# Kernel tuning notes

Measured on AMD Instinct MI355X. Metric: run time of the kernel, lower is better.

Reference implementation:

```python
import jax, jax.numpy as jnp
import numpy as np

B, L, T = 64, 256, 800
NMEL, PRE, ARNN, DRNN, ENC, ATT, NF, K = 80, 256, 512, 512, 512, 128, 32, 31
ZP = 0.1  # zoneout prob (eval-mode expected-value interpolation)


def setup_inputs() -> dict:
    key = jax.random.key(0)
    ks = iter(jax.random.split(key, 32))
    def p(shape, s=0.05):
        return jax.random.normal(next(ks), shape, dtype=jnp.float32) * s
    inp = {
        'encoder_out': jax.random.normal(next(ks), (B, L, ENC), dtype=jnp.float32),
        'lengths': jax.random.randint(next(ks), (B,), L // 2, L + 1),
        'mels': jax.random.normal(next(ks), (B, T, NMEL), dtype=jnp.float32),
        # prenet: 3 bias-free linears with relu (eval: dropout off)
        'Wp1': p((PRE, NMEL)), 'Wp2': p((PRE, PRE)), 'Wp3': p((PRE, PRE)),
        # attention LSTMCell: input = prenet_dim + enc = 768
        'aWih': p((4 * ARNN, PRE + ENC)), 'aWhh': p((4 * ARNN, ARNN)),
        'abih': jnp.zeros((4 * ARNN,)), 'abhh': jnp.zeros((4 * ARNN,)),
        # decoder LSTMCell: input = att_rnn + enc = 1024
        'dWih': p((4 * DRNN, ARNN + ENC)), 'dWhh': p((4 * DRNN, DRNN)),
        'dbih': jnp.zeros((4 * DRNN,)), 'dbhh': jnp.zeros((4 * DRNN,)),
        # location-sensitive attention (all bias-free)
        'Wq': p((ATT, ARNN)), 'Wm': p((ATT, ENC)),
        'Wconv': p((NF, 2, K)), 'Wloc': p((ATT, NF)), 'v': p((1, ATT)),
        # output projection + gate
        'Wout': p((NMEL, DRNN + ENC)), 'bout': jnp.zeros((NMEL,)),
        'Wgate': p((1, DRNN + ENC)), 'bgate': jnp.zeros((1,)),
    }
    return inp


def _lstm(x, h, c, Wih, Whh, bih, bhh):
    g = x @ Wih.T + h @ Whh.T + (bih + bhh)
    i, f, gg, o = jnp.split(g, 4, axis=-1)
    c2 = jax.nn.sigmoid(f) * c + jax.nn.sigmoid(i) * jnp.tanh(gg)
    return jax.nn.sigmoid(o) * jnp.tanh(c2), c2


def _zoneout(new, old):
    return ZP * old + (1.0 - ZP) * new


def decoder_forward(encoder_out, lengths, mels, Wp1, Wp2, Wp3,
                    aWih, aWhh, abih, abhh, dWih, dWhh, dbih, dbhh,
                    Wq, Wm, Wconv, Wloc, v, Wout, bout, Wgate, bgate):
    b, l, _ = encoder_out.shape
    t = mels.shape[1]
    processed_memory = encoder_out @ Wm.T                       # (B,L,ATT)
    mask = jnp.arange(l)[None, :] >= lengths[:, None]           # True = padded
    # teacher forcing inputs: shift mels right by one zero frame
    dec_in = jnp.concatenate(
        [jnp.zeros((b, 1, NMEL), encoder_out.dtype), mels[:, :t - 1]], axis=1)
    xs = jnp.swapaxes(dec_in, 0, 1)                             # (T,B,NMEL)

    def step(carry, frame):
        ah, ac, dh, dc, ctx, aw, aws = carry
        x = jax.nn.relu(jax.nn.relu(jax.nn.relu(frame @ Wp1.T) @ Wp2.T) @ Wp3.T)
        ah2, ac2 = _lstm(jnp.concatenate([x, ctx], -1), ah, ac, aWih, aWhh, abih, abhh)
        ah2, ac2 = _zoneout(ah2, ah), _zoneout(ac2, ac)
        # location features: conv over (B,2,L)
        aw_cat = jnp.stack([aw, aws], axis=1)
        loc = jax.lax.conv_general_dilated(
            aw_cat, Wconv, window_strides=(1,), padding=[((K - 1) // 2,) * 2],
            dimension_numbers=('NCH', 'OIH', 'NCH'))                # (B,NF,L)
        ploc = jnp.swapaxes(loc, 1, 2) @ Wloc.T                      # (B,L,ATT)
        e = jnp.tanh(ah2[:, None, :] @ Wq.T + processed_memory + ploc)
        energies = jnp.squeeze(e @ v.T, -1)                          # (B,L)
        energies = jnp.where(mask, jnp.float32(-1e9), energies)
        w = jax.nn.softmax(energies, axis=-1)
        ctx2 = jnp.einsum('bl,ble->be', w, encoder_out)
        aws2 = aws + w
        dh2, dc2 = _lstm(jnp.concatenate([ah2, ctx2], -1), dh, dc, dWih, dWhh, dbih, dbhh)
        dh2, dc2 = _zoneout(dh2, dh), _zoneout(dc2, dc)
        dhc = jnp.concatenate([dh2, ctx2], axis=-1)
        mel = dhc @ Wout.T + bout
        gate = jnp.squeeze(dhc @ Wgate.T + bgate, -1)
        return (ah2, ac2, dh2, dc2, ctx2, w, aws2), (mel, gate, w)

    z = lambda *s: jnp.zeros(s, encoder_out.dtype)
    carry0 = (z(b, ARNN), z(b, ARNN), z(b, DRNN), z(b, DRNN), z(b, ENC), z(b, l), z(b, l))
    _, (mel_t, gate_t, align_t) = jax.lax.scan(step, carry0, xs)
    return (jnp.swapaxes(mel_t, 0, 1),      # (B,T,NMEL)
            jnp.swapaxes(gate_t, 0, 1),     # (B,T)
            jnp.swapaxes(align_t, 0, 1))    # (B,T,L)


def reference(encoder_out, lengths, mels, Wp1, Wp2, Wp3,
              aWih, aWhh, abih, abhh, dWih, dWhh, dbih, dbhh,
              Wq, Wm, Wconv, Wloc, v, Wout, bout, Wgate, bgate):
    return decoder_forward(encoder_out, lengths, mels, Wp1, Wp2, Wp3,
                           aWih, aWhh, abih, abhh, dWih, dWhh, dbih, dbhh,
                           Wq, Wm, Wconv, Wloc, v, Wout, bout, Wgate, bgate)
```

## Files before the change

kernel.cpp:

```cpp
#include <hip/hip_runtime.h>


#define DEV_INLINE __device__ __forceinline__

constexpr int TB = 800;

constexpr size_t PMT_O = 0;
constexpr size_t GDT_O = 2097152;
constexpr size_t ENG_O = 2228224;
constexpr size_t WQT_O = 2244608;
constexpr size_t AH_O  = 2310144;
constexpr size_t AC_O  = 2375680;
constexpr size_t DH_O  = 2441216;
constexpr size_t DC_O  = 2506752;
constexpr size_t CTX_O = 2572288;
constexpr size_t AW_O  = 2637824;
constexpr size_t AWS_O = 2670592;
constexpr size_t XB_O  = 2703360;

constexpr size_t MEL_O  = 0;
constexpr size_t GATE_O = 4096000;
constexpr size_t ALG_O  = 4147200;

DEV_INLINE float sigf(float x)     { return 1.0f / (1.0f + __expf(-x)); }
DEV_INLINE float tanhfast(float x) { float e = __expf(2.0f * x); return 1.0f - 2.0f / (e + 1.0f); }

template<int NO>
DEV_INLINE void gseg(float* __restrict__ acc,
                     const float* __restrict__ inT,
                     const float* __restrict__ W, const int ldw, const int wcol0,
                     const int* __restrict__ rows, const int segk0, const int seglen,
                     const int ks, const int ke, const int lane)
{
  const int a0 = ks > segk0 ? ks : segk0;
  const int a1 = (ke < segk0 + seglen) ? ke : (segk0 + seglen);
  if (a0 >= a1) return;
  const float* __restrict__ ip = inT + (size_t)(a0 - segk0) * 64 + lane;
  const int n = a1 - a0;
  const float* wp[NO];
#pragma unroll
  for (int j = 0; j < NO; ++j)
    wp[j] = W + (size_t)rows[j] * ldw + (wcol0 + (a0 - segk0));
  for (int k = 0; k < n; k += 4) {
    const float x0 = ip[(k + 0) * 64];
    const float x1 = ip[(k + 1) * 64];
    const float x2 = ip[(k + 2) * 64];
    const float x3 = ip[(k + 3) * 64];
#pragma unroll
    for (int j = 0; j < NO; ++j)
      acc[j] += x0 * wp[j][k] + x1 * wp[j][k + 1] + x2 * wp[j][k + 2] + x3 * wp[j][k + 3];
  }
}

__global__ __launch_bounds__(256) void init_kernel(const float* __restrict__ Wq,
                                                   float* __restrict__ ws)
{
  const int i = blockIdx.x * 256 + threadIdx.x;
  {
    const int k = i >> 7, a = i & 127;
    ws[WQT_O + i] = Wq[a * 512 + k];
  }
  for (size_t idx = i; idx < 393216; idx += 65536)
    ws[AH_O + idx] = 0.0f;
}

__global__ __launch_bounds__(256) void prenet_kernel(const float* __restrict__ mels,
                                                     const float* __restrict__ Wp1,
                                                     const float* __restrict__ Wp2,
                                                     const float* __restrict__ Wp3,
                                                     float* __restrict__ xb, int t0)
{
  __shared__ float smem[16384];
  const int t = t0 + blockIdx.x;
  const int tid = threadIdx.x;
  const int lane = tid & 63;
  const int wv = __builtin_amdgcn_readfirstlane(tid >> 6);

  if (t == 0) {
    for (int i = tid; i < 5200; i += 256) smem[i] = 0.0f;
  } else {
    for (int i = tid; i < 5120; i += 256) {
      const int b = i / 80, k = i - b * 80;
      smem[k * 65 + b] = mels[((size_t)b * TB + (t - 1)) * 80 + k];
    }
  }
  __syncthreads();

  float va[8][8];
#pragma unroll
  for (int g = 0; g < 8; ++g) {
    const int u0 = wv * 64 + g * 8;
    float acc[8] = {};
    for (int k = 0; k < 80; ++k) {
      const float x = smem[k * 65 + lane];
#pragma unroll
      for (int j = 0; j < 8; ++j) acc[j] += x * Wp1[(u0 + j) * 80 + k];
    }
#pragma unroll
    for (int j = 0; j < 8; ++j) va[g][j] = fmaxf(acc[j], 0.0f);
  }
  __syncthreads();
#pragma unroll
  for (int g = 0; g < 8; ++g)
#pragma unroll
    for (int j = 0; j < 8; ++j) smem[(wv * 64 + g * 8 + j) * 64 + lane] = va[g][j];
  __syncthreads();

#pragma unroll
  for (int g = 0; g < 8; ++g) {
    const int u0 = wv * 64 + g * 8;
    float acc[8] = {};
    for (int k = 0; k < 256; ++k) {
      const float x = smem[k * 64 + lane];
#pragma unroll
      for (int j = 0; j < 8; ++j) acc[j] += x * Wp2[(u0 + j) * 256 + k];
    }
#pragma unroll
    for (int j = 0; j < 8; ++j) va[g][j] = fmaxf(acc[j], 0.0f);
  }
  __syncthreads();
#pragma unroll
  for (int g = 0; g < 8; ++g)
#pragma unroll
    for (int j = 0; j < 8; ++j) smem[(wv * 64 + g * 8 + j) * 64 + lane] = va[g][j];
  __syncthreads();

#pragma unroll
  for (int g = 0; g < 8; ++g) {
    const int u0 = wv * 64 + g * 8;
    float acc[8] = {};
    for (int k = 0; k < 256; ++k) {
      const float x = smem[k * 64 + lane];
#pragma unroll
      for (int j = 0; j < 8; ++j) acc[j] += x * Wp3[(u0 + j) * 256 + k];
    }
#pragma unroll
    for (int j = 0; j < 8; ++j)
      xb[((size_t)blockIdx.x * 256 + (u0 + j)) * 64 + lane] = fmaxf(acc[j], 0.0f);
  }
}

__global__ __launch_bounds__(256) void pm_kernel(const float* __restrict__ enc,
                                                 const float* __restrict__ Wm,
                                                 float* __restrict__ pmT)
{
  __shared__ float encL[64 * 129];
  const int b = blockIdx.x >> 2;
  const int l0 = (blockIdx.x & 3) * 64;
  const int tid = threadIdx.x;
  const int lane = tid & 63;
  const int wv = __builtin_amdgcn_readfirstlane(tid >> 6);

  float acc[4][8];
#pragma unroll
  for (int ai = 0; ai < 4; ++ai)
#pragma unroll
    for (int j = 0; j < 8; ++j) acc[ai][j] = 0.0f;

  for (int kc = 0; kc < 4; ++kc) {
    __syncthreads();
    for (int i = tid; i < 64 * 128; i += 256) {
      const int l = i >> 7, k = i & 127;
      encL[l * 129 + k] = enc[((size_t)b * 256 + l0 + l) * 512 + kc * 128 + k];
    }
    __syncthreads();
#pragma unroll
    for (int ai = 0; ai < 4; ++ai) {
      const int agrp = (ai * 4 + wv) * 8;
      for (int k = 0; k < 128; ++k) {
        const float x = encL[lane * 129 + k];
#pragma unroll
        for (int j = 0; j < 8; ++j)
          acc[ai][j] += x * Wm[(size_t)(agrp + j) * 512 + kc * 128 + k];
      }
    }
  }
#pragma unroll
  for (int ai = 0; ai < 4; ++ai) {
    const int agrp = (ai * 4 + wv) * 8;
#pragma unroll
    for (int j = 0; j < 8; ++j)
      pmT[((size_t)b * 128 + agrp + j) * 256 + l0 + lane] = acc[ai][j];
  }
}

__global__ __launch_bounds__(256) void k_alstm(
    const float* __restrict__ xt,  const float* __restrict__ ctx_i,
    const float* __restrict__ ah_i, const float* __restrict__ ac_i,
    float* __restrict__ ah_o, float* __restrict__ ac_o,
    const float* __restrict__ dh_i,
    const float* __restrict__ aWih, const float* __restrict__ aWhh,
    const float* __restrict__ abih, const float* __restrict__ abhh,
    const float* __restrict__ Wout, const float* __restrict__ bout,
    const float* __restrict__ Wgate, const float* __restrict__ bgate,
    float* __restrict__ out, int t, int do_a, int do_m)
{
  __shared__ float sm[2048];
  const int tid = threadIdx.x;
  const int blk = blockIdx.x;
  const int lane = tid & 63;
  const int wv = __builtin_amdgcn_readfirstlane(tid >> 6);

  if (blk < 256) {
    if (!do_a) return;
    const int u0 = blk * 2;
    int rows[8];
#pragma unroll
    for (int j = 0; j < 8; ++j) rows[j] = u0 + (j >> 2) + 512 * (j & 3);
    float acc[8] = {};
    const int ks = wv * 320, ke = ks + 320;
    gseg<8>(acc, xt,    aWih, 768, 0,   rows, 0,   256, ks, ke, lane);
    gseg<8>(acc, ctx_i, aWih, 768, 256, rows, 256, 512, ks, ke, lane);
    gseg<8>(acc, ah_i,  aWhh, 512, 0,   rows, 768, 512, ks, ke, lane);
#pragma unroll
    for (int j = 0; j < 8; ++j) sm[(wv * 8 + j) * 64 + lane] = acc[j];
    __syncthreads();
    if (tid < 128) {
      const int m = tid & 63, uq = tid >> 6;
      const int u = u0 + uq;
      float g[4];
#pragma unroll
      for (int q = 0; q < 4; ++q) {
        const int j = uq * 4 + q;
        const int row = u + 512 * q;
        g[q] = sm[j * 64 + m] + sm[(8 + j) * 64 + m] + sm[(16 + j) * 64 + m] + sm[(24 + j) * 64 + m]
             + abih[row] + abhh[row];
      }
      const float co = ac_i[u * 64 + m], ho = ah_i[u * 64 + m];
      const float c2 = sigf(g[1]) * co + sigf(g[0]) * tanhfast(g[2]);
      const float h2 = sigf(g[3]) * tanhfast(c2);
      ah_o[u * 64 + m] = 0.1f * ho + 0.9f * h2;
      ac_o[u * 64 + m] = 0.1f * co + 0.9f * c2;
    }
  } else if (do_m && blk < 277) {
    if (blk < 276) {
      const int c0 = (blk - 256) * 4;
      int rows[4] = {c0, c0 + 1, c0 + 2, c0 + 3};
      float acc[4] = {};
      const int ks = wv * 256, ke = ks + 256;
      gseg<4>(acc, dh_i,  Wout, 1024, 0,   rows, 0,   512, ks, ke, lane);
      gseg<4>(acc, ctx_i, Wout, 1024, 512, rows, 512, 512, ks, ke, lane);
#pragma unroll
      for (int j = 0; j < 4; ++j) sm[(wv * 4 + j) * 64 + lane] = acc[j];
      __syncthreads();
      {
        const int m = tid & 63, c = tid >> 6;
        const float val = sm[c * 64 + m] + sm[(4 + c) * 64 + m] + sm[(8 + c) * 64 + m] + sm[(12 + c) * 64 + m]
                        + bout[c0 + c];
        out[MEL_O + ((size_t)m * TB + (t - 1)) * 80 + c0 + c] = val;
      }
    } else {
      float acc[1] = {};
      int rows1[1] = {0};
      const int ks = wv * 256, ke = ks + 256;
      gseg<1>(acc, dh_i,  Wgate, 1024, 0,   rows1, 0,   512, ks, ke, lane);
      gseg<1>(acc, ctx_i, Wgate, 1024, 512, rows1, 512, 512, ks, ke, lane);
      sm[wv * 64 + lane] = acc[0];
      __syncthreads();
      if (tid < 64) {
        const float val = sm[tid] + sm[64 + tid] + sm[128 + tid] + sm[192 + tid] + bgate[0];
        out[GATE_O + (size_t)tid * TB + (t - 1)] = val;
      }
    }
  }
}

__global__ __launch_bounds__(256) void k_energy(
    const float* __restrict__ ah2,  const float* __restrict__ dh_i,
    const float* __restrict__ aw_i, const float* __restrict__ aws_i,
    const float* __restrict__ pmT,  const float* __restrict__ wqT,
    float* __restrict__ gdT, float* __restrict__ eng,
    const float* __restrict__ dWih, const float* __restrict__ dWhh,
    const float* __restrict__ dbih, const float* __restrict__ dbhh,
    const float* __restrict__ Wconv, const float* __restrict__ Wloc,
    const float* __restrict__ v, const int* __restrict__ len)
{
  __shared__ float sm[3584];
  const int tid = threadIdx.x;
  const int blk = blockIdx.x;
  const int lane = tid & 63;
  const int wv = __builtin_amdgcn_readfirstlane(tid >> 6);

  if (blk < 256) {
    const int u0 = blk * 2;
    int rows[8];
#pragma unroll
    for (int j = 0; j < 8; ++j) rows[j] = u0 + (j >> 2) + 512 * (j & 3);
    float acc[8] = {};
    const int ks = wv * 256, ke = ks + 256;
    gseg<8>(acc, ah2,  dWih, 1024, 0, rows, 0,   512, ks, ke, lane);
    gseg<8>(acc, dh_i, dWhh, 512,  0, rows, 512, 512, ks, ke, lane);
#pragma unroll
    for (int j = 0; j < 8; ++j) sm[(wv * 8 + j) * 64 + lane] = acc[j];
    __syncthreads();
    if (tid < 128) {
      const int m = tid & 63, uq = tid >> 6;
      const int u = u0 + uq;
#pragma unroll
      for (int q = 0; q < 4; ++q) {
        const int j = uq * 4 + q;
        const int row = u + 512 * q;
        gdT[(size_t)row * 64 + m] =
            sm[j * 64 + m] + sm[(8 + j) * 64 + m] + sm[(16 + j) * 64 + m] + sm[(24 + j) * 64 + m]
          + dbih[row] + dbhh[row];
      }
    }
  } else {
    const int eb = blk - 256;
    const int b = eb >> 2;
    const int l0 = (eb & 3) * 64;
    float* qL   = sm;
    float* a2L  = sm + 128;
    float* awL  = sm + 640;
    float* awsL = sm + 928;
    float* locL = sm + 1216;
    float* pr   = sm + 3328;

    for (int k = tid; k < 512; k += 256) a2L[k] = ah2[(size_t)k * 64 + b];
    if (tid < 15) { awL[tid] = 0.0f; awsL[tid] = 0.0f; awL[271 + tid] = 0.0f; awsL[271 + tid] = 0.0f; }
    awL[15 + tid]  = aw_i[b * 256 + tid];
    awsL[15 + tid] = aws_i[b * 256 + tid];
    __syncthreads();
    {
      const int a = tid & 127, h = tid >> 7;
      float qp = 0.0f;
      const float* wq = wqT + (size_t)(h * 256) * 128 + a;
      const float* xv = a2L + h * 256;
      for (int k = 0; k < 256; k += 4)
        qp += wq[(k + 0) * 128] * xv[k + 0] + wq[(k + 1) * 128] * xv[k + 1]
            + wq[(k + 2) * 128] * xv[k + 2] + wq[(k + 3) * 128] * xv[k + 3];
      locL[h * 128 + a] = qp;
    }
    __syncthreads();
    if (tid < 128) qL[tid] = locL[tid] + locL[128 + tid];
    __syncthreads();
    {
      float awv[31], awsv[31];
#pragma unroll
      for (int k = 0; k < 31; ++k) { awv[k] = awL[l0 + lane + k]; awsv[k] = awsL[l0 + lane + k]; }
      const int f0 = wv * 8;
      for (int f = f0; f < f0 + 8; ++f) {
        const float* wc = Wconv + f * 62;
        float lf = 0.0f;
#pragma unroll
        for (int k = 0; k < 31; ++k) lf += awv[k] * wc[k] + awsv[k] * wc[31 + k];
        locL[lane * 33 + f] = lf;
      }
    }
    __syncthreads();
    {
      float locv[32];
#pragma unroll
      for (int f = 0; f < 32; ++f) locv[f] = locL[lane * 33 + f];
      float part = 0.0f;
      const int a0 = wv * 32;
      const float* pmp = pmT + (size_t)b * 128 * 256 + l0 + lane;
      for (int a = a0; a < a0 + 32; ++a) {
        float s = qL[a] + pmp[(size_t)a * 256];
        const float* wl = Wloc + a * 32;
#pragma unroll
        for (int f = 0; f < 32; ++f) s += locv[f] * wl[f];
        part += v[a] * tanhfast(s);
      }
      pr[wv * 64 + lane] = part;
    }
    __syncthreads();
    if (tid < 64) {
      float e = pr[tid] + pr[64 + tid] + pr[128 + tid] + pr[192 + tid];
      const int l = l0 + tid;
      if (l >= len[b]) e = -1e9f;
      eng[b * 256 + l] = e;
    }
  }
}

__global__ __launch_bounds__(256) void k_ctx(
    const float* __restrict__ eng, const float* __restrict__ enc,
    const float* __restrict__ aws_i,
    float* __restrict__ ctx_o, float* __restrict__ aw_o, float* __restrict__ aws_o,
    float* __restrict__ out, int t)
{
  __shared__ float sm[896];
  const int tid = threadIdx.x;
  const int lane = tid & 63;
  const int wv = __builtin_amdgcn_readfirstlane(tid >> 6);
  const int b = blockIdx.x >> 2;
  const int ec = blockIdx.x & 3;
  const int e0 = ec * 128;
  float* eL = sm;
  float* wL = sm + 256;
  float* red = sm + 512;
  float* partL = sm + 640;

  eL[tid] = eng[b * 256 + tid];
  __syncthreads();
  float vv = eL[tid];
  for (int mm = 32; mm >= 1; mm >>= 1) vv = fmaxf(vv, __shfl_xor(vv, mm, 64));
  if (lane == 0) red[wv] = vv;
  __syncthreads();
  const float mx = fmaxf(fmaxf(red[0], red[1]), fmaxf(red[2], red[3]));
  const float pex = __expf(eL[tid] - mx);
  wL[tid] = pex;
  float ss = pex;
  for (int mm = 32; mm >= 1; mm >>= 1) ss += __shfl_xor(ss, mm, 64);
  if (lane == 0) red[4 + wv] = ss;
  __syncthreads();
  const float inv = 1.0f / (red[4] + red[5] + red[6] + red[7]);
  {
    const int e_i = tid & 127, lh = tid >> 7;
    float cp = 0.0f;
    const float* ep = enc + ((size_t)b * 256 + lh * 128) * 512 + e0 + e_i;
    for (int l = 0; l < 128; ++l) cp += wL[lh * 128 + l] * ep[(size_t)l * 512];
    partL[lh * 128 + e_i] = cp;
  }
  __syncthreads();
  if (tid < 128) ctx_o[(size_t)(e0 + tid) * 64 + b] = (partL[tid] + partL[128 + tid]) * inv;
  if (ec == 0) {
    const float w = wL[tid] * inv;
    aw_o[b * 256 + tid] = w;
    aws_o[b * 256 + tid] = aws_i[b * 256 + tid] + w;
    out[ALG_O + ((size_t)b * TB + t) * 256 + tid] = w;
  }
}

__global__ __launch_bounds__(256) void k_dfin(
    const float* __restrict__ ctx_o, const float* __restrict__ gdT,
    const float* __restrict__ dh_i,  const float* __restrict__ dc_i,
    float* __restrict__ dh_o, float* __restrict__ dc_o,
    const float* __restrict__ dWih)
{
  __shared__ float sm[2048];
  const int tid = threadIdx.x;
  const int lane = tid & 63;
  const int wv = __builtin_amdgcn_readfirstlane(tid >> 6);
  const int u0 = blockIdx.x * 2;
  int rows[8];
#pragma unroll
  for (int j = 0; j < 8; ++j) rows[j] = u0 + (j >> 2) + 512 * (j & 3);
  float acc[8] = {};
  const int ks = wv * 128, ke = ks + 128;
  gseg<8>(acc, ctx_o, dWih, 1024, 512, rows, 0, 512, ks, ke, lane);
#pragma unroll
  for (int j = 0; j < 8; ++j) sm[(wv * 8 + j) * 64 + lane] = acc[j];
  __syncthreads();
  if (tid < 128) {
    const int m = tid & 63, uq = tid >> 6;
    const int u = u0 + uq;
    float g[4];
#pragma unroll
    for (int q = 0; q < 4; ++q) {
      const int j = uq * 4 + q;
      const int row = u + 512 * q;
      g[q] = sm[j * 64 + m] + sm[(8 + j) * 64 + m] + sm[(16 + j) * 64 + m] + sm[(24 + j) * 64 + m]
           + gdT[(size_t)row * 64 + m];
    }
    const float co = dc_i[u * 64 + m], ho = dh_i[u * 64 + m];
    const float c2 = sigf(g[1]) * co + sigf(g[0]) * tanhfast(g[2]);
    const float h2 = sigf(g[3]) * tanhfast(c2);
    dh_o[u * 64 + m] = 0.1f * ho + 0.9f * h2;
    dc_o[u * 64 + m] = 0.1f * co + 0.9f * c2;
  }
}

extern "C" void kernel_launch(void* const* d_in, const int* in_sizes, int n_in,
                              void* d_out, int out_size, void* d_ws, size_t ws_size,
                              hipStream_t stream)
{
  (void)in_sizes; (void)n_in; (void)out_size;
  const float* enc   = (const float*)d_in[0];
  const int*   len   = (const int*)  d_in[1];
  const float* mels  = (const float*)d_in[2];
  const float* Wp1   = (const float*)d_in[3];
  const float* Wp2   = (const float*)d_in[4];
  const float* Wp3   = (const float*)d_in[5];
  const float* aWih  = (const float*)d_in[6];
  const float* aWhh  = (const float*)d_in[7];
  const float* abih  = (const float*)d_in[8];
  const float* abhh  = (const float*)d_in[9];
  const float* dWih  = (const float*)d_in[10];
  const float* dWhh  = (const float*)d_in[11];
  const float* dbih  = (const float*)d_in[12];
  const float* dbhh  = (const float*)d_in[13];
  const float* Wq    = (const float*)d_in[14];
  const float* Wm    = (const float*)d_in[15];
  const float* Wconv = (const float*)d_in[16];
  const float* Wloc  = (const float*)d_in[17];
  const float* vv    = (const float*)d_in[18];
  const float* Wout  = (const float*)d_in[19];
  const float* bout  = (const float*)d_in[20];
  const float* Wgate = (const float*)d_in[21];
  const float* bgate = (const float*)d_in[22];

  float* ws  = (float*)d_ws;
  float* out = (float*)d_out;

  const size_t need_big = (XB_O + (size_t)TB * 16384) * 4;
  const int CH = (ws_size >= need_big) ? TB : 64;

  init_kernel<<<256, 256, 0, stream>>>(Wq, ws);
  pm_kernel<<<256, 256, 0, stream>>>(enc, Wm, ws + PMT_O);

  for (int t = 0; t <= TB; ++t) {
    if (t < TB && (t % CH) == 0) {
      const int nt = (TB - t) < CH ? (TB - t) : CH;
      prenet_kernel<<<nt, 256, 0, stream>>>(mels, Wp1, Wp2, Wp3, ws + XB_O, t);
    }
    const int cur = t & 1;
    const float* xt = ws + XB_O + (size_t)(t % CH) * 16384;
    float* ah_i = ws + AH_O  + (size_t)cur * 32768;  float* ah_o = ws + AH_O  + (size_t)(cur ^ 1) * 32768;
    float* ac_i = ws + AC_O  + (size_t)cur * 32768;  float* ac_o = ws + AC_O  + (size_t)(cur ^ 1) * 32768;
    float* dh_i = ws + DH_O  + (size_t)cur * 32768;  float* dh_o = ws + DH_O  + (size_t)(cur ^ 1) * 32768;
    float* dc_i = ws + DC_O  + (size_t)cur * 32768;  float* dc_o = ws + DC_O  + (size_t)(cur ^ 1) * 32768;
    float* ctx_i = ws + CTX_O + (size_t)cur * 32768; float* ctx_o = ws + CTX_O + (size_t)(cur ^ 1) * 32768;
    float* aw_i = ws + AW_O  + (size_t)cur * 16384;  float* aw_o = ws + AW_O  + (size_t)(cur ^ 1) * 16384;
    float* aws_i = ws + AWS_O + (size_t)cur * 16384; float* aws_o = ws + AWS_O + (size_t)(cur ^ 1) * 16384;

    k_alstm<<<277, 256, 0, stream>>>(xt, ctx_i, ah_i, ac_i, ah_o, ac_o, dh_i,
                                     aWih, aWhh, abih, abhh,
                                     Wout, bout, Wgate, bgate,
                                     out, t, (t < TB) ? 1 : 0, (t > 0) ? 1 : 0);
    if (t == TB) break;
    k_energy<<<512, 256, 0, stream>>>(ah_o, dh_i, aw_i, aws_i,
                                      ws + PMT_O, ws + WQT_O, ws + GDT_O, ws + ENG_O,
                                      dWih, dWhh, dbih, dbhh, Wconv, Wloc, vv, len);
    k_ctx<<<256, 256, 0, stream>>>(ws + ENG_O, enc, aws_i, ctx_o, aw_o, aws_o, out, t);
    k_dfin<<<256, 256, 0, stream>>>(ctx_o, ws + GDT_O, dh_i, dc_i, dh_o, dc_o, dWih);
  }
}
```

Before: 87.46 ms.

## Replace per-step kernel launches with a persistent kernel using grid barriers

Swaps the roughly 3200 per-timestep kernel launches for one persistent 256-block kernel. Its blocks split the work by role (attention LSTM, decoder gates, energy and context, mel and gate, prenet stages) and meet at a software global barrier built on an atomic counter, two barriers per step. The prenet is now computed one step ahead inside the loop instead of as a bulk precompute, and the location-conv features are staged separately. This targets launch overhead and inter-kernel gaps on a latency-bound recurrence. It relies on all 256 blocks being co-resident and adds atomic spin-wait cost at every barrier.

```diff
diff --git a/kernel.cpp b/kernel.cpp
--- a/kernel.cpp
+++ b/kernel.cpp
@@ -5,18 +5,22 @@
 
 constexpr int TB = 800;
 
-constexpr size_t PMT_O = 0;
-constexpr size_t GDT_O = 2097152;
-constexpr size_t ENG_O = 2228224;
-constexpr size_t WQT_O = 2244608;
-constexpr size_t AH_O  = 2310144;
-constexpr size_t AC_O  = 2375680;
-constexpr size_t DH_O  = 2441216;
-constexpr size_t DC_O  = 2506752;
-constexpr size_t CTX_O = 2572288;
-constexpr size_t AW_O  = 2637824;
-constexpr size_t AWS_O = 2670592;
-constexpr size_t XB_O  = 2703360;
+constexpr size_t PMT_O  = 0;
+constexpr size_t GDT_O  = 2097152;
+constexpr size_t WQT_O  = 2228224;
+constexpr size_t LOCF_O = 2293760;
+constexpr size_t Y1_O   = 2818048;
+constexpr size_t Y2_O   = 2834432;
+constexpr size_t XR_O   = 2850816;
+constexpr size_t AH_O   = 2883584;
+constexpr size_t AC_O   = 2949120;
+constexpr size_t DH_O   = 3014656;
+constexpr size_t DC_O   = 3080192;
+constexpr size_t CTX_O  = 3145728;
+constexpr size_t AW_O   = 3211264;
+constexpr size_t AWS_O  = 3244032;
+constexpr size_t BAR_O  = 3276800;
+constexpr size_t ZERO_N = 983296;
 
 constexpr size_t MEL_O  = 0;
 constexpr size_t GATE_O = 4096000;
@@ -24,6 +28,28 @@
 
 DEV_INLINE float sigf(float x)     { return 1.0f / (1.0f + __expf(-x)); }
 DEV_INLINE float tanhfast(float x) { float e = __expf(2.0f * x); return 1.0f - 2.0f / (e + 1.0f); }
+
+struct Params {
+  const float* enc; const int* len; const float* mels;
+  const float* Wp1; const float* Wp2; const float* Wp3;
+  const float* aWih; const float* aWhh; const float* abih; const float* abhh;
+  const float* dWih; const float* dWhh; const float* dbih; const float* dbhh;
+  const float* Wconv; const float* Wloc; const float* v;
+  const float* Wout; const float* bout; const float* Wgate; const float* bgate;
+  float* ws; float* out;
+};
+
+DEV_INLINE void gbar(unsigned* cnt, unsigned target)
+{
+  __syncthreads();
+  __threadfence();
+  if (threadIdx.x == 0) {
+    atomicAdd(cnt, 1u);
+    while (atomicAdd(cnt, 0u) < target) __builtin_amdgcn_s_sleep(8);
+  }
+  __syncthreads();
+  __threadfence();
+}
 
 template<int NO>
 DEV_INLINE void gseg(float* __restrict__ acc,
@@ -60,18 +86,18 @@
     const int k = i >> 7, a = i & 127;
     ws[WQT_O + i] = Wq[a * 512 + k];
   }
-  for (size_t idx = i; idx < 393216; idx += 65536)
-    ws[AH_O + idx] = 0.0f;
+  for (size_t idx = i; idx < ZERO_N; idx += 65536)
+    ws[LOCF_O + idx] = 0.0f;
 }
 
 __global__ __launch_bounds__(256) void prenet_kernel(const float* __restrict__ mels,
                                                      const float* __restrict__ Wp1,
                                                      const float* __restrict__ Wp2,
                                                      const float* __restrict__ Wp3,
-                                                     float* __restrict__ xb, int t0)
+                                                     float* __restrict__ xb)
 {
   __shared__ float smem[16384];
-  const int t = t0 + blockIdx.x;
+  const int t = blockIdx.x;
   const int tid = threadIdx.x;
   const int lane = tid & 63;
   const int wv = __builtin_amdgcn_readfirstlane(tid >> 6);
@@ -136,7 +162,7 @@
     }
 #pragma unroll
     for (int j = 0; j < 8; ++j)
-      xb[((size_t)blockIdx.x * 256 + (u0 + j)) * 64 + lane] = fmaxf(acc[j], 0.0f);
+      xb[((size_t)t * 256 + (u0 + j)) * 64 + lane] = fmaxf(acc[j], 0.0f);
   }
 }
 
@@ -184,262 +210,71 @@
   }
 }
 
-__global__ __launch_bounds__(256) void k_alstm(
-    const float* __restrict__ xt,  const float* __restrict__ ctx_i,
-    const float* __restrict__ ah_i, const float* __restrict__ ac_i,
-    float* __restrict__ ah_o, float* __restrict__ ac_o,
-    const float* __restrict__ dh_i,
-    const float* __restrict__ aWih, const float* __restrict__ aWhh,
-    const float* __restrict__ abih, const float* __restrict__ abhh,
-    const float* __restrict__ Wout, const float* __restrict__ bout,
-    const float* __restrict__ Wgate, const float* __restrict__ bgate,
-    float* __restrict__ out, int t, int do_a, int do_m)
-{
-  __shared__ float sm[2048];
-  const int tid = threadIdx.x;
-  const int blk = blockIdx.x;
-  const int lane = tid & 63;
-  const int wv = __builtin_amdgcn_readfirstlane(tid >> 6);
-
-  if (blk < 256) {
-    if (!do_a) return;
-    const int u0 = blk * 2;
-    int rows[8];
-#pragma unroll
-    for (int j = 0; j < 8; ++j) rows[j] = u0 + (j >> 2) + 512 * (j & 3);
-    float acc[8] = {};
-    const int ks = wv * 320, ke = ks + 320;
-    gseg<8>(acc, xt,    aWih, 768, 0,   rows, 0,   256, ks, ke, lane);
-    gseg<8>(acc, ctx_i, aWih, 768, 256, rows, 256, 512, ks, ke, lane);
-    gseg<8>(acc, ah_i,  aWhh, 512, 0,   rows, 768, 512, ks, ke, lane);
-#pragma unroll
-    for (int j = 0; j < 8; ++j) sm[(wv * 8 + j) * 64 + lane] = acc[j];
-    __syncthreads();
-    if (tid < 128) {
-      const int m = tid & 63, uq = tid >> 6;
-      const int u = u0 + uq;
-      float g[4];
-#pragma unroll
-      for (int q = 0; q < 4; ++q) {
-        const int j = uq * 4 + q;
-        const int row = u + 512 * q;
-        g[q] = sm[j * 64 + m] + sm[(8 + j) * 64 + m] + sm[(16 + j) * 64 + m] + sm[(24 + j) * 64 + m]
-             + abih[row] + abhh[row];
-      }
-      const float co = ac_i[u * 64 + m], ho = ah_i[u * 64 + m];
-      const float c2 = sigf(g[1]) * co + sigf(g[0]) * tanhfast(g[2]);
-      const float h2 = sigf(g[3]) * tanhfast(c2);
-      ah_o[u * 64 + m] = 0.1f * ho + 0.9f * h2;
-      ac_o[u * 64 + m] = 0.1f * co + 0.9f * c2;
-    }
-  } else if (do_m && blk < 277) {
-    if (blk < 276) {
-      const int c0 = (blk - 256) * 4;
-      int rows[4] = {c0, c0 + 1, c0 + 2, c0 + 3};
-      float acc[4] = {};
-      const int ks = wv * 256, ke = ks + 256;
-      gseg<4>(acc, dh_i,  Wout, 1024, 0,   rows, 0,   512, ks, ke, lane);
-      gseg<4>(acc, ctx_i, Wout, 1024, 512, rows, 512, 512, ks, ke, lane);
-#pragma unroll
-      for (int j = 0; j < 4; ++j) sm[(wv * 4 + j) * 64 + lane] = acc[j];
-      __syncthreads();
-      {
-        const int m = tid & 63, c = tid >> 6;
-        const float val = sm[c * 64 + m] + sm[(4 + c) * 64 + m] + sm[(8 + c) * 64 + m] + sm[(12 + c) * 64 + m]
-                        + bout[c0 + c];
-        out[MEL_O + ((size_t)m * TB + (t - 1)) * 80 + c0 + c] = val;
-      }
-    } else {
-      float acc[1] = {};
-      int rows1[1] = {0};
-      const int ks = wv * 256, ke = ks + 256;
-      gseg<1>(acc, dh_i,  Wgate, 1024, 0,   rows1, 0,   512, ks, ke, lane);
-      gseg<1>(acc, ctx_i, Wgate, 1024, 512, rows1, 512, 512, ks, ke, lane);
-      sm[wv * 64 + lane] = acc[0];
-      __syncthreads();
-      if (tid < 64) {
-        const float val = sm[tid] + sm[64 + tid] + sm[128 + tid] + sm[192 + tid] + bgate[0];
-        out[GATE_O + (size_t)tid * TB + (t - 1)] = val;
-      }
-    }
-  }
-}
-
-__global__ __launch_bounds__(256) void k_energy(
-    const float* __restrict__ ah2,  const float* __restrict__ dh_i,
-    const float* __restrict__ aw_i, const float* __restrict__ aws_i,
-    const float* __restrict__ pmT,  const float* __restrict__ wqT,
-    float* __restrict__ gdT, float* __restrict__ eng,
-    const float* __restrict__ dWih, const float* __restrict__ dWhh,
-    const float* __restrict__ dbih, const float* __restrict__ dbhh,
-    const float* __restrict__ Wconv, const float* __restrict__ Wloc,
-    const float* __restrict__ v, const int* __restrict__ len)
-{
-  __shared__ float sm[3584];
-  const int tid = threadIdx.x;
-  const int blk = blockIdx.x;
-  const int lane = tid & 63;
-  const int wv = __builtin_amdgcn_readfirstlane(tid >> 6);
-
-  if (blk < 256) {
-    const int u0 = blk * 2;
-    int rows[8];
-#pragma unroll
-    for (int j = 0; j < 8; ++j) rows[j] = u0 + (j >> 2) + 512 * (j & 3);
-    float acc[8] = {};
-    const int ks = wv * 256, ke = ks + 256;
-    gseg<8>(acc, ah2,  dWih, 1024, 0, rows, 0,   512, ks, ke, lane);
-    gseg<8>(acc, dh_i, dWhh, 512,  0, rows, 512, 512, ks, ke, lane);
-#pragma unroll
-    for (int j = 0; j < 8; ++j) sm[(wv * 8 + j) * 64 + lane] = acc[j];
-    __syncthreads();
-    if (tid < 128) {
-      const int m = tid & 63, uq = tid >> 6;
-      const int u = u0 + uq;
-#pragma unroll
-      for (int q = 0; q < 4; ++q) {
-        const int j = uq * 4 + q;
-        const int row = u + 512 * q;
-        gdT[(size_t)row * 64 + m] =
-            sm[j * 64 + m] + sm[(8 + j) * 64 + m] + sm[(16 + j) * 64 + m] + sm[(24 + j) * 64 + m]
-          + dbih[row] + dbhh[row];
-      }
-    }
-  } else {
-    const int eb = blk - 256;
-    const int b = eb >> 2;
-    const int l0 = (eb & 3) * 64;
-    float* qL   = sm;
-    float* a2L  = sm + 128;
-    float* awL  = sm + 640;
-    float* awsL = sm + 928;
-    float* locL = sm + 1216;
-    float* pr   = sm + 3328;
-
-    for (int k = tid; k < 512; k += 256) a2L[k] = ah2[(size_t)k * 64 + b];
-    if (tid < 15) { awL[tid] = 0.0f; awsL[tid] = 0.0f; awL[271 + tid] = 0.0f; awsL[271 + tid] = 0.0f; }
-    awL[15 + tid]  = aw_i[b * 256 + tid];
-    awsL[15 + tid] = aws_i[b * 256 + tid];
-    __syncthreads();
-    {
-      const int a = tid & 127, h = tid >> 7;
-      float qp = 0.0f;
-      const float* wq = wqT + (size_t)(h * 256) * 128 + a;
-      const float* xv = a2L + h * 256;
-      for (int k = 0; k < 256; k += 4)
-        qp += wq[(k + 0) * 128] * xv[k + 0] + wq[(k + 1) * 128] * xv[k + 1]
-            + wq[(k + 2) * 128] * xv[k + 2] + wq[(k + 3) * 128] * xv[k + 3];
-      locL[h * 128 + a] = qp;
-    }
-    __syncthreads();
-    if (tid < 128) qL[tid] = locL[tid] + locL[128 + tid];
-    __syncthreads();
-    {
-      float awv[31], awsv[31];
-#pragma unroll
-      for (int k = 0; k < 31; ++k) { awv[k] = awL[l0 + lane + k]; awsv[k] = awsL[l0 + lane + k]; }
-      const int f0 = wv * 8;
-      for (int f = f0; f < f0 + 8; ++f) {
-        const float* wc = Wconv + f * 62;
-        float lf = 0.0f;
-#pragma unroll
-        for (int k = 0; k < 31; ++k) lf += awv[k] * wc[k] + awsv[k] * wc[31 + k];
-        locL[lane * 33 + f] = lf;
-      }
-    }
-    __syncthreads();
-    {
-      float locv[32];
-#pragma unroll
-      for (int f = 0; f < 32; ++f) locv[f] = locL[lane * 33 + f];
-      float part = 0.0f;
-      const int a0 = wv * 32;
-      const float* pmp = pmT + (size_t)b * 128 * 256 + l0 + lane;
-      for (int a = a0; a < a0 + 32; ++a) {
-        float s = qL[a] + pmp[(size_t)a * 256];
-        const float* wl = Wloc + a * 32;
-#pragma unroll
-        for (int f = 0; f < 32; ++f) s += locv[f] * wl[f];
-        part += v[a] * tanhfast(s);
-      }
-      pr[wv * 64 + lane] = part;
-    }
-    __syncthreads();
-    if (tid < 64) {
-      float e = pr[tid] + pr[64 + tid] + pr[128 + tid] + pr[192 + tid];
-      const int l = l0 + tid;
-      if (l >= len[b]) e = -1e9f;
-      eng[b * 256 + l] = e;
-    }
-  }
-}
-
-__global__ __launch_bounds__(256) void k_ctx(
-    const float* __restrict__ eng, const float* __restrict__ enc,
-    const float* __restrict__ aws_i,
-    float* __restrict__ ctx_o, float* __restrict__ aw_o, float* __restrict__ aws_o,
-    float* __restrict__ out, int t)
-{
-  __shared__ float sm[896];
-  const int tid = threadIdx.x;
-  const int lane = tid & 63;
-  const int wv = __builtin_amdgcn_readfirstlane(tid >> 6);
-  const int b = blockIdx.x >> 2;
-  const int ec = blockIdx.x & 3;
-  const int e0 = ec * 128;
-  float* eL = sm;
-  float* wL = sm + 256;
-  float* red = sm + 512;
-  float* partL = sm + 640;
-
-  eL[tid] = eng[b * 256 + tid];
-  __syncthreads();
-  float vv = eL[tid];
-  for (int mm = 32; mm >= 1; mm >>= 1) vv = fmaxf(vv, __shfl_xor(vv, mm, 64));
-  if (lane == 0) red[wv] = vv;
-  __syncthreads();
-  const float mx = fmaxf(fmaxf(red[0], red[1]), fmaxf(red[2], red[3]));
-  const float pex = __expf(eL[tid] - mx);
-  wL[tid] = pex;
-  float ss = pex;
-  for (int mm = 32; mm >= 1; mm >>= 1) ss += __shfl_xor(ss, mm, 64);
-  if (lane == 0) red[4 + wv] = ss;
-  __syncthreads();
-  const float inv = 1.0f / (red[4] + red[5] + red[6] + red[7]);
-  {
-    const int e_i = tid & 127, lh = tid >> 7;
-    float cp = 0.0f;
-    const float* ep = enc + ((size_t)b * 256 + lh * 128) * 512 + e0 + e_i;
-    for (int l = 0; l < 128; ++l) cp += wL[lh * 128 + l] * ep[(size_t)l * 512];
-    partL[lh * 128 + e_i] = cp;
-  }
-  __syncthreads();
-  if (tid < 128) ctx_o[(size_t)(e0 + tid) * 64 + b] = (partL[tid] + partL[128 + tid]) * inv;
-  if (ec == 0) {
-    const float w = wL[tid] * inv;
-    aw_o[b * 256 + tid] = w;
-    aws_o[b * 256 + tid] = aws_i[b * 256 + tid] + w;
-    out[ALG_O + ((size_t)b * TB + t) * 256 + tid] = w;
-  }
-}
-
-__global__ __launch_bounds__(256) void k_dfin(
-    const float* __restrict__ ctx_o, const float* __restrict__ gdT,
-    const float* __restrict__ dh_i,  const float* __restrict__ dc_i,
-    float* __restrict__ dh_o, float* __restrict__ dc_o,
-    const float* __restrict__ dWih)
-{
-  __shared__ float sm[2048];
-  const int tid = threadIdx.x;
-  const int lane = tid & 63;
-  const int wv = __builtin_amdgcn_readfirstlane(tid >> 6);
-  const int u0 = blockIdx.x * 2;
+
+DEV_INLINE void f_alstm(int u, int tid, int lane, int wv,
+                        const float* __restrict__ xt, const float* __restrict__ ctx,
+                        const float* __restrict__ ah_i, const float* __restrict__ ac_i,
+                        float* __restrict__ ah_o, float* __restrict__ ac_o,
+                        const Params& p, float* sm)
+{
+  int rows[4] = {u, u + 512, u + 1024, u + 1536};
+  float acc[4] = {};
+  const int ks = wv * 320, ke = ks + 320;
+  gseg<4>(acc, xt,   p.aWih, 768, 0,   rows, 0,   256, ks, ke, lane);
+  gseg<4>(acc, ctx,  p.aWih, 768, 256, rows, 256, 512, ks, ke, lane);
+  gseg<4>(acc, ah_i, p.aWhh, 512, 0,   rows, 768, 512, ks, ke, lane);
+#pragma unroll
+  for (int j = 0; j < 4; ++j) sm[(wv * 4 + j) * 64 + lane] = acc[j];
+  __syncthreads();
+  if (tid < 64) {
+    const int m = tid;
+    float g[4];
+#pragma unroll
+    for (int q = 0; q < 4; ++q)
+      g[q] = sm[q * 64 + m] + sm[(4 + q) * 64 + m] + sm[(8 + q) * 64 + m] + sm[(12 + q) * 64 + m]
+           + p.abih[u + 512 * q] + p.abhh[u + 512 * q];
+    const float co = ac_i[u * 64 + m], ho = ah_i[u * 64 + m];
+    const float c2 = sigf(g[1]) * co + sigf(g[0]) * tanhfast(g[2]);
+    const float h2 = sigf(g[3]) * tanhfast(c2);
+    ah_o[u * 64 + m] = 0.1f * ho + 0.9f * h2;
+    ac_o[u * 64 + m] = 0.1f * co + 0.9f * c2;
+  }
+}
+
+DEV_INLINE void f_dgates(int u, int tid, int lane, int wv,
+                         const float* __restrict__ ah, const float* __restrict__ dh,
+                         float* __restrict__ gdT, const Params& p, float* sm)
+{
+  int rows[4] = {u, u + 512, u + 1024, u + 1536};
+  float acc[4] = {};
+  const int ks = wv * 256, ke = ks + 256;
+  gseg<4>(acc, ah, p.dWih, 1024, 0, rows, 0,   512, ks, ke, lane);
+  gseg<4>(acc, dh, p.dWhh, 512,  0, rows, 512, 512, ks, ke, lane);
+#pragma unroll
+  for (int j = 0; j < 4; ++j) sm[(wv * 4 + j) * 64 + lane] = acc[j];
+  __syncthreads();
+  if (tid < 64) {
+    const int m = tid;
+#pragma unroll
+    for (int q = 0; q < 4; ++q)
+      gdT[(size_t)(u + 512 * q) * 64 + m] =
+          sm[q * 64 + m] + sm[(4 + q) * 64 + m] + sm[(8 + q) * 64 + m] + sm[(12 + q) * 64 + m]
+        + p.dbih[u + 512 * q] + p.dbhh[u + 512 * q];
+  }
+}
+
+DEV_INLINE void f_dfin(int u0, int tid, int lane, int wv,
+                       const float* __restrict__ ctx, const float* __restrict__ gdT,
+                       const float* __restrict__ dh_p, const float* __restrict__ dc_p,
+                       float* __restrict__ dh_o, float* __restrict__ dc_o,
+                       const Params& p, float* sm)
+{
   int rows[8];
 #pragma unroll
   for (int j = 0; j < 8; ++j) rows[j] = u0 + (j >> 2) + 512 * (j & 3);
   float acc[8] = {};
   const int ks = wv * 128, ke = ks + 128;
-  gseg<8>(acc, ctx_o, dWih, 1024, 512, rows, 0, 512, ks, ke, lane);
+  gseg<8>(acc, ctx, p.dWih, 1024, 512, rows, 0, 512, ks, ke, lane);
 #pragma unroll
   for (int j = 0; j < 8; ++j) sm[(wv * 8 + j) * 64 + lane] = acc[j];
   __syncthreads();
@@ -450,11 +285,10 @@
 #pragma unroll
     for (int q = 0; q < 4; ++q) {
       const int j = uq * 4 + q;
-      const int row = u + 512 * q;
       g[q] = sm[j * 64 + m] + sm[(8 + j) * 64 + m] + sm[(16 + j) * 64 + m] + sm[(24 + j) * 64 + m]
-           + gdT[(size_t)row * 64 + m];
-    }
-    const float co = dc_i[u * 64 + m], ho = dh_i[u * 64 + m];
+           + gdT[(size_t)(u + 512 * q) * 64 + m];
+    }
+    const float co = dc_p[u * 64 + m], ho = dh_p[u * 64 + m];
     const float c2 = sigf(g[1]) * co + sigf(g[0]) * tanhfast(g[2]);
     const float h2 = sigf(g[3]) * tanhfast(c2);
     dh_o[u * 64 + m] = 0.1f * ho + 0.9f * h2;
@@ -462,68 +296,297 @@
   }
 }
 
+DEV_INLINE void f_mel(int c0, int tid, int lane, int wv, int tm1,
+                      const float* __restrict__ dh, const float* __restrict__ ctx,
+                      const Params& p, float* sm)
+{
+  int rows[4] = {c0, c0 + 1, c0 + 2, c0 + 3};
+  float acc[4] = {};
+  const int ks = wv * 256, ke = ks + 256;
+  gseg<4>(acc, dh,  p.Wout, 1024, 0,   rows, 0,   512, ks, ke, lane);
+  gseg<4>(acc, ctx, p.Wout, 1024, 512, rows, 512, 512, ks, ke, lane);
+#pragma unroll
+  for (int j = 0; j < 4; ++j) sm[(wv * 4 + j) * 64 + lane] = acc[j];
+  __syncthreads();
+  {
+    const int m = tid & 63, c = tid >> 6;
+    const float val = sm[c * 64 + m] + sm[(4 + c) * 64 + m] + sm[(8 + c) * 64 + m] + sm[(12 + c) * 64 + m]
+                    + p.bout[c0 + c];
+    p.out[MEL_O + ((size_t)m * TB + tm1) * 80 + c0 + c] = val;
+  }
+}
+
+DEV_INLINE void f_gate(int tid, int lane, int wv, int tm1,
+                       const float* __restrict__ dh, const float* __restrict__ ctx,
+                       const Params& p, float* sm)
+{
+  float acc[1] = {};
+  int rows1[1] = {0};
+  const int ks = wv * 256, ke = ks + 256;
+  gseg<1>(acc, dh,  p.Wgate, 1024, 0,   rows1, 0,   512, ks, ke, lane);
+  gseg<1>(acc, ctx, p.Wgate, 1024, 512, rows1, 512, 512, ks, ke, lane);
+  sm[wv * 64 + lane] = acc[0];
+  __syncthreads();
+  if (tid < 64) {
+    const float val = sm[tid] + sm[64 + tid] + sm[128 + tid] + sm[192 + tid] + p.bgate[0];
+    p.out[GATE_O + (size_t)tid * TB + tm1] = val;
+  }
+}
+
+DEV_INLINE void f_conv(int b, int tid,
+                       const float* __restrict__ aw, const float* __restrict__ aws,
+                       float* __restrict__ locF, const Params& p, float* sm)
+{
+  float* awL  = sm;
+  float* awsL = sm + 290;
+  if (tid < 15) { awL[tid] = 0.0f; awsL[tid] = 0.0f; awL[271 + tid] = 0.0f; awsL[271 + tid] = 0.0f; }
+  awL[15 + tid]  = aw[b * 256 + tid];
+  awsL[15 + tid] = aws[b * 256 + tid];
+  __syncthreads();
+  float awv[31], awsv[31];
+#pragma unroll
+  for (int k = 0; k < 31; ++k) { awv[k] = awL[tid + k]; awsv[k] = awsL[tid + k]; }
+  float* dst = locF + ((size_t)b * 256 + tid) * 32;
+  for (int f = 0; f < 32; ++f) {
+    const float* wc = p.Wconv + f * 62;
+    float lf = 0.0f;
+#pragma unroll
+    for (int k = 0; k < 31; ++k) lf += awv[k] * wc[k] + awsv[k] * wc[31 + k];
+    dst[f] = lf;
+  }
+  __syncthreads();
+}
+
+DEV_INLINE void f_energy(int b, int t, int tid, int lane, int wv,
+                         const float* __restrict__ ah, const float* __restrict__ aws_p,
+                         float* __restrict__ ctx_o, float* __restrict__ aw_o,
+                         float* __restrict__ aws_o,
+                         const float* __restrict__ pmT, const float* __restrict__ wqT,
+                         const float* __restrict__ locF, const Params& p, float* sm)
+{
+  float* ahL = sm;
+  float* qpL = sm + 512;
+  float* qL  = sm + 768;
+  float* red = sm + 896;
+  float* wL  = sm + 912;
+  ahL[tid]       = ah[(size_t)tid * 64 + b];
+  ahL[tid + 256] = ah[(size_t)(tid + 256) * 64 + b];
+  __syncthreads();
+  {
+    const int a = tid & 127, h = tid >> 7;
+    float qp = 0.0f;
+    const float* wq = wqT + (size_t)(h * 256) * 128 + a;
+    const float* xv = ahL + h * 256;
+    for (int k = 0; k < 256; k += 4)
+      qp += wq[(k + 0) * 128] * xv[k + 0] + wq[(k + 1) * 128] * xv[k + 1]
+          + wq[(k + 2) * 128] * xv[k + 2] + wq[(k + 3) * 128] * xv[k + 3];
+    qpL[tid] = qp;
+  }
+  __syncthreads();
+  if (tid < 128) qL[tid] = qpL[tid] + qpL[128 + tid];
+  __syncthreads();
+
+  float locv[32];
+  {
+    const float4* lf4 = (const float4*)(locF + ((size_t)b * 256 + tid) * 32);
+#pragma unroll
+    for (int i = 0; i < 8; ++i) {
+      float4 x = lf4[i];
+      locv[4*i] = x.x; locv[4*i+1] = x.y; locv[4*i+2] = x.z; locv[4*i+3] = x.w;
+    }
+  }
+  float part = 0.0f;
+  const float* pmp = pmT + (size_t)b * 32768 + tid;
+#pragma unroll 2
+  for (int a = 0; a < 128; ++a) {
+    float s = qL[a] + pmp[(size_t)a * 256];
+    const float* wl = p.Wloc + a * 32;
+#pragma unroll
+    for (int f = 0; f < 32; ++f) s += locv[f] * wl[f];
+    part += p.v[a] * tanhfast(s);
+  }
+  if (tid >= p.len[b]) part = -1e9f;
+
+  float mv = part;
+  for (int mm = 32; mm >= 1; mm >>= 1) mv = fmaxf(mv, __shfl_xor(mv, mm, 64));
+  if (lane == 0) red[wv] = mv;
+  __syncthreads();
+  const float mx = fmaxf(fmaxf(red[0], red[1]), fmaxf(red[2], red[3]));
+  const float pex = __expf(part - mx);
+  float ssum = pex;
+  for (int mm = 32; mm >= 1; mm >>= 1) ssum += __shfl_xor(ssum, mm, 64);
+  if (lane == 0) red[8 + wv] = ssum;
+  __syncthreads();
+  const float inv = 1.0f / (red[8] + red[9] + red[10] + red[11]);
+  const float w = pex * inv;
+  wL[tid] = w;
+  aw_o[b * 256 + tid]  = w;
+  aws_o[b * 256 + tid] = aws_p[b * 256 + tid] + w;
+  p.out[ALG_O + ((size_t)b * TB + t) * 256 + tid] = w;
+  __syncthreads();
+
+  float c0 = 0.0f, c1 = 0.0f;
+  const float* ep = p.enc + (size_t)b * 256 * 512;
+  for (int l = 0; l < 256; ++l) {
+    const float wv_ = wL[l];
+    c0 += wv_ * ep[(size_t)l * 512 + tid];
+    c1 += wv_ * ep[(size_t)l * 512 + tid + 256];
+  }
+  ctx_o[(size_t)tid * 64 + b]         = c0;
+  ctx_o[(size_t)(tid + 256) * 64 + b] = c1;
+}
+
+DEV_INLINE void f_pn1(int blkL, int frame, int lane, int wv,
+                      const Params& p, float* __restrict__ y1)
+{
+  const int u0 = blkL * 32 + wv * 8;
+  float acc[8] = {};
+  const float* mp = p.mels + ((size_t)lane * TB + frame) * 80;
+  for (int k = 0; k < 80; ++k) {
+    const float x = mp[k];
+#pragma unroll
+    for (int j = 0; j < 8; ++j) acc[j] += x * p.Wp1[(u0 + j) * 80 + k];
+  }
+#pragma unroll
+  for (int j = 0; j < 8; ++j) y1[(size_t)(u0 + j) * 64 + lane] = fmaxf(acc[j], 0.0f);
+}
+
+DEV_INLINE void f_pnmid(int blkL, int lane, int wv,
+                        const float* __restrict__ yin, const float* __restrict__ W,
+                        float* __restrict__ yout)
+{
+  const int u0 = blkL * 32 + wv * 8;
+  float acc[8] = {};
+  for (int k = 0; k < 256; ++k) {
+    const float x = yin[(size_t)k * 64 + lane];
+#pragma unroll
+    for (int j = 0; j < 8; ++j) acc[j] += x * W[(u0 + j) * 256 + k];
+  }
+#pragma unroll
+  for (int j = 0; j < 8; ++j) yout[(size_t)(u0 + j) * 64 + lane] = fmaxf(acc[j], 0.0f);
+}
+
+__global__ __launch_bounds__(256) void persist_kernel(Params p)
+{
+  __shared__ float sm[2048];
+  const int tid = threadIdx.x, blk = blockIdx.x;
+  const int lane = tid & 63;
+  const int wv = __builtin_amdgcn_readfirstlane(tid >> 6);
+
+  float* ws   = p.ws;
+  float* pmT  = ws + PMT_O;
+  float* gdT  = ws + GDT_O;
+  float* wqT  = ws + WQT_O;
+  float* locF = ws + LOCF_O;
+  float* y1   = ws + Y1_O;
+  float* y2   = ws + Y2_O;
+  float* xr   = ws + XR_O;
+  float* AH[2]  = {ws + AH_O,  ws + AH_O  + 32768};
+  float* AC[2]  = {ws + AC_O,  ws + AC_O  + 32768};
+  float* DH[2]  = {ws + DH_O,  ws + DH_O  + 32768};
+  float* DC[2]  = {ws + DC_O,  ws + DC_O  + 32768};
+  float* CTX[2] = {ws + CTX_O, ws + CTX_O + 32768};
+  float* AW[2]  = {ws + AW_O,  ws + AW_O  + 16384};
+  float* AWS[2] = {ws + AWS_O, ws + AWS_O + 16384};
+  unsigned* cnt = (unsigned*)(ws + BAR_O);
+  unsigned nbar = 0;
+
+  if (blk < 8) f_pn1(blk, 1, lane, wv, p, y1);
+  ++nbar; gbar(cnt, nbar * 256u);
+
+  if (blk < 128) {
+    for (int i = 0; i < 4; ++i) {
+      f_alstm(blk * 4 + i, tid, lane, wv, xr, CTX[1], AH[1], AC[1], AH[0], AC[0], p, sm);
+      __syncthreads();
+    }
+  } else if (blk >= 208 && blk < 216) {
+    f_pnmid(blk - 208, lane, wv, y1, p.Wp2, y2);
+  }
+  ++nbar; gbar(cnt, nbar * 256u);
+
+  for (int t = 0; t < TB; ++t) {
+    const int cur = t & 1, prv = cur ^ 1;
+    if (blk < 128) {
+      for (int i = 0; i < 4; ++i) {
+        f_dgates(blk * 4 + i, tid, lane, wv, AH[cur], DH[prv], gdT, p, sm);
+        __syncthreads();
+      }
+    } else if (blk < 192) {
+      f_energy(blk - 128, t, tid, lane, wv, AH[cur], AWS[prv],
+               CTX[cur], AW[cur], AWS[cur], pmT, wqT, locF, p, sm);
+    } else if (blk < 212) {
+      if (t > 0) f_mel((blk - 192) * 4, tid, lane, wv, t - 1, DH[prv], CTX[prv], p, sm);
+    } else if (blk == 212) {
+      if (t > 0) f_gate(tid, lane, wv, t - 1, DH[prv], CTX[prv], p, sm);
+    } else if (blk < 221) {
+      if (t <= 796) f_pn1(blk - 213, t + 2, lane, wv, p, y1);
+    } else if (blk < 229) {
+      if (t <= 797) f_pnmid(blk - 221, lane, wv, y2, p.Wp3, xr + (size_t)cur * 16384);
+    }
+    ++nbar; gbar(cnt, nbar * 256u);
+
+    if (blk < 128) {
+      if (t < TB - 1) {
+        for (int i = 0; i < 4; ++i) {
+          f_alstm(blk * 4 + i, tid, lane, wv, xr + (size_t)prv * 16384, CTX[cur],
+                  AH[cur], AC[cur], AH[prv], AC[prv], p, sm);
+          __syncthreads();
+        }
+      }
+    } else if (blk < 192) {
+      for (int i = 0; i < 4; ++i) {
+        f_dfin((blk - 128) * 8 + i * 2, tid, lane, wv, CTX[cur], gdT, DH[prv], DC[prv],
+               DH[cur], DC[cur], p, sm);
+        __syncthreads();
+      }
+    } else if (blk < 208) {
+      if (t < TB - 1)
+        for (int i = 0; i < 4; ++i)
+          f_conv((blk - 192) * 4 + i, tid, AW[cur], AWS[cur], locF, p, sm);
+    } else if (blk < 216) {
+      if (t <= 796) f_pnmid(blk - 208, lane, wv, y1, p.Wp2, y2);
+    }
+    ++nbar; gbar(cnt, nbar * 256u);
+  }
+  if (blk < 20)       f_mel(blk * 4, tid, lane, wv, TB - 1, DH[1], CTX[1], p, sm);
+  else if (blk == 20) f_gate(tid, lane, wv, TB - 1, DH[1], CTX[1], p, sm);
+}
+
 extern "C" void kernel_launch(void* const* d_in, const int* in_sizes, int n_in,
                               void* d_out, int out_size, void* d_ws, size_t ws_size,
                               hipStream_t stream)
 {
-  (void)in_sizes; (void)n_in; (void)out_size;
-  const float* enc   = (const float*)d_in[0];
-  const int*   len   = (const int*)  d_in[1];
-  const float* mels  = (const float*)d_in[2];
-  const float* Wp1   = (const float*)d_in[3];
-  const float* Wp2   = (const float*)d_in[4];
-  const float* Wp3   = (const float*)d_in[5];
-  const float* aWih  = (const float*)d_in[6];
-  const float* aWhh  = (const float*)d_in[7];
-  const float* abih  = (const float*)d_in[8];
-  const float* abhh  = (const float*)d_in[9];
-  const float* dWih  = (const float*)d_in[10];
-  const float* dWhh  = (const float*)d_in[11];
-  const float* dbih  = (const float*)d_in[12];
-  const float* dbhh  = (const float*)d_in[13];
-  const float* Wq    = (const float*)d_in[14];
-  const float* Wm    = (const float*)d_in[15];
-  const float* Wconv = (const float*)d_in[16];
-  const float* Wloc  = (const float*)d_in[17];
-  const float* vv    = (const float*)d_in[18];
-  const float* Wout  = (const float*)d_in[19];
-  const float* bout  = (const float*)d_in[20];
-  const float* Wgate = (const float*)d_in[21];
-  const float* bgate = (const float*)d_in[22];
-
-  float* ws  = (float*)d_ws;
-  float* out = (float*)d_out;
-
-  const size_t need_big = (XB_O + (size_t)TB * 16384) * 4;
-  const int CH = (ws_size >= need_big) ? TB : 64;
-
-  init_kernel<<<256, 256, 0, stream>>>(Wq, ws);
-  pm_kernel<<<256, 256, 0, stream>>>(enc, Wm, ws + PMT_O);
-
-  for (int t = 0; t <= TB; ++t) {
-    if (t < TB && (t % CH) == 0) {
-      const int nt = (TB - t) < CH ? (TB - t) : CH;
-      prenet_kernel<<<nt, 256, 0, stream>>>(mels, Wp1, Wp2, Wp3, ws + XB_O, t);
-    }
-    const int cur = t & 1;
-    const float* xt = ws + XB_O + (size_t)(t % CH) * 16384;
-    float* ah_i = ws + AH_O  + (size_t)cur * 32768;  float* ah_o = ws + AH_O  + (size_t)(cur ^ 1) * 32768;
-    float* ac_i = ws + AC_O  + (size_t)cur * 32768;  float* ac_o = ws + AC_O  + (size_t)(cur ^ 1) * 32768;
-    float* dh_i = ws + DH_O  + (size_t)cur * 32768;  float* dh_o = ws + DH_O  + (size_t)(cur ^ 1) * 32768;
-    float* dc_i = ws + DC_O  + (size_t)cur * 32768;  float* dc_o = ws + DC_O  + (size_t)(cur ^ 1) * 32768;
-    float* ctx_i = ws + CTX_O + (size_t)cur * 32768; float* ctx_o = ws + CTX_O + (size_t)(cur ^ 1) * 32768;
-    float* aw_i = ws + AW_O  + (size_t)cur * 16384;  float* aw_o = ws + AW_O  + (size_t)(cur ^ 1) * 16384;
-    float* aws_i = ws + AWS_O + (size_t)cur * 16384; float* aws_o = ws + AWS_O + (size_t)(cur ^ 1) * 16384;
-
-    k_alstm<<<277, 256, 0, stream>>>(xt, ctx_i, ah_i, ac_i, ah_o, ac_o, dh_i,
-                                     aWih, aWhh, abih, abhh,
-                                     Wout, bout, Wgate, bgate,
-                                     out, t, (t < TB) ? 1 : 0, (t > 0) ? 1 : 0);
-    if (t == TB) break;
-    k_energy<<<512, 256, 0, stream>>>(ah_o, dh_i, aw_i, aws_i,
-                                      ws + PMT_O, ws + WQT_O, ws + GDT_O, ws + ENG_O,
-                                      dWih, dWhh, dbih, dbhh, Wconv, Wloc, vv, len);
-    k_ctx<<<256, 256, 0, stream>>>(ws + ENG_O, enc, aws_i, ctx_o, aw_o, aws_o, out, t);
-    k_dfin<<<256, 256, 0, stream>>>(ctx_o, ws + GDT_O, dh_i, dc_i, dh_o, dc_o, dWih);
-  }
-}
+  (void)in_sizes; (void)n_in; (void)out_size; (void)ws_size;
+  Params P;
+  P.enc   = (const float*)d_in[0];
+  P.len   = (const int*)  d_in[1];
+  P.mels  = (const float*)d_in[2];
+  P.Wp1   = (const float*)d_in[3];
+  P.Wp2   = (const float*)d_in[4];
+  P.Wp3   = (const float*)d_in[5];
+  P.aWih  = (const float*)d_in[6];
+  P.aWhh  = (const float*)d_in[7];
+  P.abih  = (const float*)d_in[8];
+  P.abhh  = (const float*)d_in[9];
+  P.dWih  = (const float*)d_in[10];
+  P.dWhh  = (const float*)d_in[11];
+  P.dbih  = (const float*)d_in[12];
+  P.dbhh  = (const float*)d_in[13];
+  const float* Wq = (const float*)d_in[14];
+  const float* Wm = (const float*)d_in[15];
+  P.Wconv = (const float*)d_in[16];
+  P.Wloc  = (const float*)d_in[17];
+  P.v     = (const float*)d_in[18];
+  P.Wout  = (const float*)d_in[19];
+  P.bout  = (const float*)d_in[20];
+  P.Wgate = (const float*)d_in[21];
+  P.bgate = (const float*)d_in[22];
+  P.ws  = (float*)d_ws;
+  P.out = (float*)d_out;
+
+  init_kernel<<<256, 256, 0, stream>>>(Wq, P.ws);
+  pm_kernel<<<256, 256, 0, stream>>>(P.enc, Wm, P.ws + PMT_O);
+  prenet_kernel<<<2, 256, 0, stream>>>(P.mels, P.Wp1, P.Wp2, P.Wp3, P.ws + XR_O);
+
+  persist_kernel<<<256, 256, 0, stream>>>(P);
+}
```

Result: slower. 189.0 ms (+116.1%).
